# Kernel optimization log

Hardware: AMD Instinct MI355X
Metric: run time of the kernel (lower is better)

Reference implementation:

```python
import jax, jax.numpy as jnp
import numpy as np

K = 4  # number of conv kernel experts in CondConv_down


def setup_inputs() -> dict:
    key = jax.random.key(0)
    ks = jax.random.split(key, 8)
    N, Cin, H, W = 8, 64, 384, 384
    Cin2, Cout4, Cout2 = Cin // 2, 128 // 4, 128 // 2  # 32, 32, 64
    return {
        "x": jax.random.normal(ks[0], (N, Cin, H, W), jnp.float32),
        # square conv: Conv2d(in=64, out=64, 3x3, stride 2, pad 1, bias)
        "sq_w": jax.random.normal(ks[1], (Cout2, Cin, 3, 3), jnp.float32) * 0.05,
        "sq_b": jnp.zeros((Cout2,), jnp.float32),
        # vertical CondConv: attention 1x1 conv (== linear on pooled feats) + K expert kernels [3,1]
        "att_w_v": jax.random.normal(ks[2], (K, Cin2), jnp.float32) * 0.1,
        "att_b_v": jnp.zeros((K,), jnp.float32),
        "w_v": jax.random.normal(ks[3], (K, Cout4, Cin2, 3, 1), jnp.float32) * 0.05,
        "bn_v_g": jnp.ones((Cout4,), jnp.float32),
        "bn_v_b": jnp.zeros((Cout4,), jnp.float32),
        # horizontal CondConv: K expert kernels [1,3]
        "att_w_h": jax.random.normal(ks[4], (K, Cin2), jnp.float32) * 0.1,
        "att_b_h": jnp.zeros((K,), jnp.float32),
        "w_h": jax.random.normal(ks[5], (K, Cout4, Cin2, 1, 3), jnp.float32) * 0.05,
        "bn_h_g": jnp.ones((Cout4,), jnp.float32),
        "bn_h_b": jnp.zeros((Cout4,), jnp.float32),
    }


def _condconv(x, att_w, att_b, w, pad):
    # Attention: global avg pool -> 1x1 conv -> sigmoid (note: sigmoid, not softmax, as in source)
    att = jax.nn.sigmoid(jnp.mean(x, axis=(2, 3)) @ att_w.T + att_b)  # [N, K]
    # Aggregate expert kernels per sample: [N, Cout, Cin, kh, kw]
    agg = jnp.einsum("nk,koihw->noihw", att, w)
    def one(xi, wi):
        return jax.lax.conv_general_dilated(
            xi[None], wi, window_strides=(2, 2),
            padding=[(pad[0], pad[0]), (pad[1], pad[1])],
            dimension_numbers=("NCHW", "OIHW", "NCHW"))[0]
    return jax.vmap(one)(x, agg)  # per-sample dynamic conv == groups=N grouped conv


def _bn(x, g, b, eps=1e-5):
    # training-mode BatchNorm2d: batch statistics over (N, H, W), biased variance
    m = jnp.mean(x, axis=(0, 2, 3), keepdims=True)
    v = jnp.var(x, axis=(0, 2, 3), keepdims=True)
    return (x - m) * jax.lax.rsqrt(v + eps) * g[None, :, None, None] + b[None, :, None, None]


def _shuffle(x, g=8):
    N, C, H, W = x.shape
    return x.reshape(N, g, C // g, H, W).transpose(0, 2, 1, 3, 4).reshape(N, C, H, W)


def reference(x, sq_w, sq_b, att_w_v, att_b_v, w_v, bn_v_g, bn_v_b,
              att_w_h, att_b_h, w_h, bn_h_g, bn_h_b):
    sq = jax.lax.conv_general_dilated(
        x, sq_w, window_strides=(2, 2), padding=[(1, 1), (1, 1)],
        dimension_numbers=("NCHW", "OIHW", "NCHW")) + sq_b[None, :, None, None]
    x1, x2 = jnp.split(x, 2, axis=1)
    v = _bn(_condconv(x1, att_w_v, att_b_v, w_v, (1, 0)), bn_v_g, bn_v_b)
    h = _bn(_condconv(x2, att_w_h, att_b_h, w_h, (0, 1)), bn_h_g, bn_h_b)
    out = jnp.concatenate([sq, v, h], axis=1)  # [N, 128, H/2, W/2]
    return _shuffle(out, 8)
```

## Files before the change

### kernel.cpp

```cpp
#include <hip/hip_runtime.h>

#define NB    8
#define HIN   384
#define WIN   384
#define HOUT  192
#define WOUT  192
#define HW_IN (HIN * WIN)
#define PLANE (HOUT * WOUT)
#define CNT_BN (NB * HOUT * WOUT)

#define WS_MEANS 0
#define WS_AGGV  512
#define WS_AGGH  25088
#define WS_SQW   49664
#define WS_STATS 86528
#define WS_BN    86656

__global__ void k_zero(float* __restrict__ ws) {
    if (threadIdx.x < 128) ws[WS_STATS + threadIdx.x] = 0.f;
}

__global__ __launch_bounds__(256) void k_means(const float* __restrict__ x,
                                               float* __restrict__ ws) {
    int bc = blockIdx.x;
    const float4* p = (const float4*)(x + (size_t)bc * HW_IN);
    float s = 0.f;
    for (int i = threadIdx.x; i < HW_IN / 4; i += 256) {
        float4 v = p[i];
        s += (v.x + v.y) + (v.z + v.w);
    }
    __shared__ float red[256];
    red[threadIdx.x] = s;
    __syncthreads();
    for (int off = 128; off > 0; off >>= 1) {
        if ((int)threadIdx.x < off) red[threadIdx.x] += red[threadIdx.x + off];
        __syncthreads();
    }
    if (threadIdx.x == 0) ws[WS_MEANS + bc] = red[0] * (1.0f / HW_IN);
}

__global__ void k_agg(const float* __restrict__ aw_v, const float* __restrict__ ab_v,
                      const float* __restrict__ wv,
                      const float* __restrict__ aw_h, const float* __restrict__ ab_h,
                      const float* __restrict__ wh, float* __restrict__ ws) {
    int n = blockIdx.x;
    __shared__ float att[8];
    if (threadIdx.x < 8) {
        int k = threadIdx.x & 3;
        int hsel = threadIdx.x >> 2;
        const float* m = ws + WS_MEANS + n * 64 + hsel * 32;
        const float* aw = hsel ? aw_h : aw_v;
        const float* ab = hsel ? ab_h : ab_v;
        float z = ab[k];
        for (int c = 0; c < 32; c++) z += m[c] * aw[k * 32 + c];
        att[threadIdx.x] = 1.0f / (1.0f + expf(-z));
    }
    __syncthreads();
    for (int i = threadIdx.x; i < 3072; i += 256) {
        int o = i & 31;
        int r = i >> 5;
        float sv = 0.f, sh = 0.f;
#pragma unroll
        for (int k = 0; k < 4; k++) {
            sv += att[k]     * wv[(k * 32 + o) * 96 + r];
            sh += att[4 + k] * wh[(k * 32 + o) * 96 + r];
        }
        ws[WS_AGGV + n * 3072 + i] = sv;
        ws[WS_AGGH + n * 3072 + i] = sh;
    }
}

__global__ void k_cvtw(const float* __restrict__ sq_w, float* __restrict__ ws) {
    int i = blockIdx.x * 256 + threadIdx.x;
    int oc = i & 63;
    int r = i >> 6;
    int c = r / 9, q = r % 9;
    ws[WS_SQW + i] = sq_w[(oc * 64 + c) * 9 + q];
}

__global__ __launch_bounds__(192) void k_sq(const float* __restrict__ x,
                                            const float* __restrict__ sq_b,
                                            const float* __restrict__ ws,
                                            float* __restrict__ out) {
    int xo = threadIdx.x;
    int yo = blockIdx.x;
    int n  = blockIdx.y;
    int ocg = blockIdx.z;
    const float* wp = ws + WS_SQW + ocg * 32;
    const float* bptr = sq_b + ocg * 32;
    float acc[32];
#pragma unroll
    for (int j = 0; j < 32; j++) acc[j] = bptr[j];
    const float* xb = x + (size_t)n * 64 * HW_IN;
    int c2 = 2 * xo;
    for (int c = 0; c < 64; c++) {
        const float* xc = xb + (size_t)c * HW_IN;
#pragma unroll
        for (int ky = 0; ky < 3; ky++) {
            int iy = 2 * yo - 1 + ky;
            if (iy >= 0) {
                const float* row = xc + (size_t)iy * WIN;
                float2 v12 = *(const float2*)(row + c2);
                float v0 = (xo > 0) ? row[c2 - 1] : 0.f;
                const float* wr = wp + (c * 9 + ky * 3) * 64;
#pragma unroll
                for (int j = 0; j < 32; j++)
                    acc[j] += v0 * wr[j] + v12.x * wr[64 + j] + v12.y * wr[128 + j];
            }
        }
    }
    size_t ob = (size_t)n * 128 * PLANE + (size_t)yo * WOUT + xo;
#pragma unroll
    for (int j = 0; j < 32; j++) {
        int ci = ocg * 32 + j;
        int co = ((ci & 15) << 3) | (ci >> 4);
        out[ob + (size_t)co * PLANE] = acc[j];
    }
}

__global__ __launch_bounds__(192) void k_vert(const float* __restrict__ x,
                                              const float* __restrict__ ws,
                                              float* __restrict__ out) {
    int xo = threadIdx.x, yo = blockIdx.x, n = blockIdx.y;
    const float* wn = ws + WS_AGGV + n * 3072;
    float acc[32];
#pragma unroll
    for (int j = 0; j < 32; j++) acc[j] = 0.f;
    const float* xb = x + (size_t)n * 64 * HW_IN;
    int c2 = 2 * xo;
    for (int c = 0; c < 32; c++) {
        const float* xc = xb + (size_t)c * HW_IN;
#pragma unroll
        for (int t = 0; t < 3; t++) {
            int iy = 2 * yo - 1 + t;
            if (iy >= 0) {
                float v = xc[(size_t)iy * WIN + c2];
                const float* wr = wn + (c * 3 + t) * 32;
#pragma unroll
                for (int j = 0; j < 32; j++) acc[j] += v * wr[j];
            }
        }
    }
    size_t ob = (size_t)n * 128 * PLANE + (size_t)yo * WOUT + xo;
#pragma unroll
    for (int j = 0; j < 32; j++) {
        int ci = 64 + j;
        int co = ((ci & 15) << 3) | (ci >> 4);
        out[ob + (size_t)co * PLANE] = acc[j];
    }
}

__global__ __launch_bounds__(192) void k_horz(const float* __restrict__ x,
                                              const float* __restrict__ ws,
                                              float* __restrict__ out) {
    int xo = threadIdx.x, yo = blockIdx.x, n = blockIdx.y;
    const float* wn = ws + WS_AGGH + n * 3072;
    float acc[32];
#pragma unroll
    for (int j = 0; j < 32; j++) acc[j] = 0.f;
    const float* xb = x + ((size_t)n * 64 + 32) * HW_IN;
    int c2 = 2 * xo;
    for (int c = 0; c < 32; c++) {
        const float* row = xb + (size_t)c * HW_IN + (size_t)(2 * yo) * WIN;
        float2 v12 = *(const float2*)(row + c2);
        float v0 = (xo > 0) ? row[c2 - 1] : 0.f;
        const float* wr = wn + c * 96;
#pragma unroll
        for (int j = 0; j < 32; j++)
            acc[j] += v0 * wr[j] + v12.x * wr[32 + j] + v12.y * wr[64 + j];
    }
    size_t ob = (size_t)n * 128 * PLANE + (size_t)yo * WOUT + xo;
#pragma unroll
    for (int j = 0; j < 32; j++) {
        int ci = 96 + j;
        int co = ((ci & 15) << 3) | (ci >> 4);
        out[ob + (size_t)co * PLANE] = acc[j];
    }
}

__global__ __launch_bounds__(256) void k_stats(const float* __restrict__ out,
                                               float* __restrict__ ws) {
    int sch = blockIdx.x;
    int n = blockIdx.y;
    int vh = sch >> 5, oc = sch & 31;
    int ci = 64 + sch;
    int co = ((ci & 15) << 3) | (ci >> 4);
    const float4* p = (const float4*)(out + (size_t)(n * 128 + co) * PLANE);
    float s = 0.f, q = 0.f;
    for (int i = threadIdx.x; i < PLANE / 4; i += 256) {
        float4 v = p[i];
        s += (v.x + v.y) + (v.z + v.w);
        q += (v.x * v.x + v.y * v.y) + (v.z * v.z + v.w * v.w);
    }
    __shared__ float rs[256], rq[256];
    rs[threadIdx.x] = s; rq[threadIdx.x] = q;
    __syncthreads();
    for (int off = 128; off > 0; off >>= 1) {
        if ((int)threadIdx.x < off) {
            rs[threadIdx.x] += rs[threadIdx.x + off];
            rq[threadIdx.x] += rq[threadIdx.x + off];
        }
        __syncthreads();
    }
    if (threadIdx.x == 0) {
        atomicAdd(&ws[WS_STATS + vh * 64 + oc], rs[0]);
        atomicAdd(&ws[WS_STATS + vh * 64 + 32 + oc], rq[0]);
    }
}

__global__ void k_bnfin(const float* __restrict__ gv, const float* __restrict__ bv,
                        const float* __restrict__ gh, const float* __restrict__ bh,
                        float* __restrict__ ws) {
    int t = threadIdx.x;
    if (t >= 64) return;
    int vh = t >> 5;
    int c = t & 31;
    const float* st = ws + WS_STATS + vh * 64;
    float mean = st[c] * (1.0f / CNT_BN);
    float var = st[32 + c] * (1.0f / CNT_BN) - mean * mean;
    float g = vh ? gh[c] : gv[c];
    float b = vh ? bh[c] : bv[c];
    float scale = g * rsqrtf(var + 1e-5f);
    float* bn = ws + WS_BN + vh * 64;
    bn[c] = scale;
    bn[32 + c] = b - mean * scale;
}

__global__ __launch_bounds__(256) void k_apply(float* __restrict__ out,
                                               const float* __restrict__ ws) {
    int sch = blockIdx.x;
    int n = blockIdx.y;
    int vh = sch >> 5, oc = sch & 31;
    int ci = 64 + sch;
    int co = ((ci & 15) << 3) | (ci >> 4);
    const float* bn = ws + WS_BN + vh * 64;
    float scale = bn[oc], shift = bn[32 + oc];
    float4* p = (float4*)(out + (size_t)(n * 128 + co) * PLANE);
    for (int i = threadIdx.x; i < PLANE / 4; i += 256) {
        float4 v = p[i];
        v.x = v.x * scale + shift;
        v.y = v.y * scale + shift;
        v.z = v.z * scale + shift;
        v.w = v.w * scale + shift;
        p[i] = v;
    }
}

extern "C" void kernel_launch(void* const* d_in, const int* in_sizes, int n_in,
                              void* d_out, int out_size, void* d_ws, size_t ws_size,
                              hipStream_t stream) {
    const float* x    = (const float*)d_in[0];
    const float* sq_w = (const float*)d_in[1];
    const float* sq_b = (const float*)d_in[2];
    const float* aw_v = (const float*)d_in[3];
    const float* ab_v = (const float*)d_in[4];
    const float* w_v  = (const float*)d_in[5];
    const float* gv   = (const float*)d_in[6];
    const float* bv   = (const float*)d_in[7];
    const float* aw_h = (const float*)d_in[8];
    const float* ab_h = (const float*)d_in[9];
    const float* w_h  = (const float*)d_in[10];
    const float* gh   = (const float*)d_in[11];
    const float* bh   = (const float*)d_in[12];
    float* out = (float*)d_out;
    float* ws = (float*)d_ws;

    hipLaunchKernelGGL(k_zero, dim3(1), dim3(128), 0, stream, ws);
    hipLaunchKernelGGL(k_means, dim3(512), dim3(256), 0, stream, x, ws);
    hipLaunchKernelGGL(k_agg, dim3(8), dim3(256), 0, stream,
                       aw_v, ab_v, w_v, aw_h, ab_h, w_h, ws);
    hipLaunchKernelGGL(k_cvtw, dim3(144), dim3(256), 0, stream, sq_w, ws);
    hipLaunchKernelGGL(k_vert, dim3(192, 8), dim3(192), 0, stream, x, ws, out);
    hipLaunchKernelGGL(k_horz, dim3(192, 8), dim3(192), 0, stream, x, ws, out);
    hipLaunchKernelGGL(k_stats, dim3(64, 8), dim3(256), 0, stream, out, ws);
    hipLaunchKernelGGL(k_bnfin, dim3(1), dim3(64), 0, stream, gv, bv, gh, bh, ws);
    hipLaunchKernelGGL(k_apply, dim3(64, 8), dim3(256), 0, stream, out, ws);
    hipLaunchKernelGGL(k_sq, dim3(192, 8, 2), dim3(192), 0, stream, x, sq_b, ws, out);
}
```

Baseline: 948.2 us.

## Compute all 64 square-conv channels per thread, merge vert/horz kernels, split means

The square conv kernel now computes all 64 output channels per thread instead of two 32-channel groups. Each input pixel is loaded once, which halves reads of x, at the cost of 64 accumulators and more register pressure. The vertical and horizontal CondConv kernels are merged into one launch with a z-dimension selector, with unroll pragmas added. The channel-mean reduction is split into 4 parts per plane combined via atomicAdd, with scaling moved into k_agg, to expose more parallelism.

```diff
diff --git a/kernel.cpp b/kernel.cpp
--- a/kernel.cpp
+++ b/kernel.cpp
@@ -17,15 +17,17 @@
 #define WS_BN    86656
 
 __global__ void k_zero(float* __restrict__ ws) {
+    for (int i = threadIdx.x; i < 512; i += 256) ws[WS_MEANS + i] = 0.f;
     if (threadIdx.x < 128) ws[WS_STATS + threadIdx.x] = 0.f;
 }
 
 __global__ __launch_bounds__(256) void k_means(const float* __restrict__ x,
                                                float* __restrict__ ws) {
     int bc = blockIdx.x;
-    const float4* p = (const float4*)(x + (size_t)bc * HW_IN);
+    int part = blockIdx.y;
+    const float4* p = (const float4*)(x + (size_t)bc * HW_IN) + part * (HW_IN / 16);
     float s = 0.f;
-    for (int i = threadIdx.x; i < HW_IN / 4; i += 256) {
+    for (int i = threadIdx.x; i < HW_IN / 16; i += 256) {
         float4 v = p[i];
         s += (v.x + v.y) + (v.z + v.w);
     }
@@ -36,7 +38,7 @@
         if ((int)threadIdx.x < off) red[threadIdx.x] += red[threadIdx.x + off];
         __syncthreads();
     }
-    if (threadIdx.x == 0) ws[WS_MEANS + bc] = red[0] * (1.0f / HW_IN);
+    if (threadIdx.x == 0) atomicAdd(&ws[WS_MEANS + bc], red[0]);
 }
 
 __global__ void k_agg(const float* __restrict__ aw_v, const float* __restrict__ ab_v,
@@ -51,8 +53,9 @@
         const float* m = ws + WS_MEANS + n * 64 + hsel * 32;
         const float* aw = hsel ? aw_h : aw_v;
         const float* ab = hsel ? ab_h : ab_v;
-        float z = ab[k];
-        for (int c = 0; c < 32; c++) z += m[c] * aw[k * 32 + c];
+        float dot = 0.f;
+        for (int c = 0; c < 32; c++) dot += m[c] * aw[k * 32 + c];
+        float z = ab[k] + dot * (1.0f / HW_IN);
         att[threadIdx.x] = 1.0f / (1.0f + expf(-z));
     }
     __syncthreads();
@@ -85,94 +88,94 @@
     int xo = threadIdx.x;
     int yo = blockIdx.x;
     int n  = blockIdx.y;
-    int ocg = blockIdx.z;
-    const float* wp = ws + WS_SQW + ocg * 32;
-    const float* bptr = sq_b + ocg * 32;
-    float acc[32];
-#pragma unroll
-    for (int j = 0; j < 32; j++) acc[j] = bptr[j];
+    const float* wp = ws + WS_SQW;
+    float acc[64];
+#pragma unroll
+    for (int j = 0; j < 64; j++) acc[j] = sq_b[j];
     const float* xb = x + (size_t)n * 64 * HW_IN;
     int c2 = 2 * xo;
+    int iy0 = 2 * yo - 1;
     for (int c = 0; c < 64; c++) {
         const float* xc = xb + (size_t)c * HW_IN;
+        float v[9];
 #pragma unroll
         for (int ky = 0; ky < 3; ky++) {
-            int iy = 2 * yo - 1 + ky;
+            int iy = iy0 + ky;
             if (iy >= 0) {
                 const float* row = xc + (size_t)iy * WIN;
                 float2 v12 = *(const float2*)(row + c2);
-                float v0 = (xo > 0) ? row[c2 - 1] : 0.f;
-                const float* wr = wp + (c * 9 + ky * 3) * 64;
-#pragma unroll
-                for (int j = 0; j < 32; j++)
-                    acc[j] += v0 * wr[j] + v12.x * wr[64 + j] + v12.y * wr[128 + j];
+                v[ky * 3 + 0] = (xo > 0) ? row[c2 - 1] : 0.f;
+                v[ky * 3 + 1] = v12.x;
+                v[ky * 3 + 2] = v12.y;
+            } else {
+                v[ky * 3 + 0] = v[ky * 3 + 1] = v[ky * 3 + 2] = 0.f;
             }
         }
+        const float* wc = wp + c * 576;
+#pragma unroll
+        for (int t = 0; t < 9; t++) {
+            float vv = v[t];
+#pragma unroll
+            for (int j = 0; j < 64; j++) acc[j] += vv * wc[t * 64 + j];
+        }
     }
     size_t ob = (size_t)n * 128 * PLANE + (size_t)yo * WOUT + xo;
 #pragma unroll
+    for (int j = 0; j < 64; j++) {
+        int co = ((j & 15) << 3) | (j >> 4);
+        out[ob + (size_t)co * PLANE] = acc[j];
+    }
+}
+
+__global__ __launch_bounds__(192) void k_vh(const float* __restrict__ x,
+                                            const float* __restrict__ ws,
+                                            float* __restrict__ out) {
+    int xo = threadIdx.x, yo = blockIdx.x, n = blockIdx.y;
+    int horz = blockIdx.z;
+    float acc[32];
+#pragma unroll
+    for (int j = 0; j < 32; j++) acc[j] = 0.f;
+    if (!horz) {
+        const float* wn = ws + WS_AGGV + n * 3072;
+        const float* xb = x + (size_t)n * 64 * HW_IN;
+        int c2 = 2 * xo;
+        int iy0 = 2 * yo - 1;
+#pragma unroll 4
+        for (int c = 0; c < 32; c++) {
+            const float* xc = xb + (size_t)c * HW_IN;
+            float v[3];
+#pragma unroll
+            for (int t = 0; t < 3; t++) {
+                int iy = iy0 + t;
+                v[t] = (iy >= 0) ? xc[(size_t)iy * WIN + c2] : 0.f;
+            }
+#pragma unroll
+            for (int t = 0; t < 3; t++) {
+                const float* wr = wn + (c * 3 + t) * 32;
+#pragma unroll
+                for (int j = 0; j < 32; j++) acc[j] += v[t] * wr[j];
+            }
+        }
+    } else {
+        const float* wn = ws + WS_AGGH + n * 3072;
+        const float* xb = x + ((size_t)n * 64 + 32) * HW_IN;
+        int c2 = 2 * xo;
+#pragma unroll 4
+        for (int c = 0; c < 32; c++) {
+            const float* row = xb + (size_t)c * HW_IN + (size_t)(2 * yo) * WIN;
+            float2 v12 = *(const float2*)(row + c2);
+            float v0 = (xo > 0) ? row[c2 - 1] : 0.f;
+            const float* wr = wn + c * 96;
+#pragma unroll
+            for (int j = 0; j < 32; j++)
+                acc[j] += v0 * wr[j] + v12.x * wr[32 + j] + v12.y * wr[64 + j];
+        }
+    }
+    int cb = horz ? 96 : 64;
+    size_t ob = (size_t)n * 128 * PLANE + (size_t)yo * WOUT + xo;
+#pragma unroll
     for (int j = 0; j < 32; j++) {
-        int ci = ocg * 32 + j;
-        int co = ((ci & 15) << 3) | (ci >> 4);
-        out[ob + (size_t)co * PLANE] = acc[j];
-    }
-}
-
-__global__ __launch_bounds__(192) void k_vert(const float* __restrict__ x,
-                                              const float* __restrict__ ws,
-                                              float* __restrict__ out) {
-    int xo = threadIdx.x, yo = blockIdx.x, n = blockIdx.y;
-    const float* wn = ws + WS_AGGV + n * 3072;
-    float acc[32];
-#pragma unroll
-    for (int j = 0; j < 32; j++) acc[j] = 0.f;
-    const float* xb = x + (size_t)n * 64 * HW_IN;
-    int c2 = 2 * xo;
-    for (int c = 0; c < 32; c++) {
-        const float* xc = xb + (size_t)c * HW_IN;
-#pragma unroll
-        for (int t = 0; t < 3; t++) {
-            int iy = 2 * yo - 1 + t;
-            if (iy >= 0) {
-                float v = xc[(size_t)iy * WIN + c2];
-                const float* wr = wn + (c * 3 + t) * 32;
-#pragma unroll
-                for (int j = 0; j < 32; j++) acc[j] += v * wr[j];
-            }
-        }
-    }
-    size_t ob = (size_t)n * 128 * PLANE + (size_t)yo * WOUT + xo;
-#pragma unroll
-    for (int j = 0; j < 32; j++) {
-        int ci = 64 + j;
-        int co = ((ci & 15) << 3) | (ci >> 4);
-        out[ob + (size_t)co * PLANE] = acc[j];
-    }
-}
-
-__global__ __launch_bounds__(192) void k_horz(const float* __restrict__ x,
-                                              const float* __restrict__ ws,
-                                              float* __restrict__ out) {
-    int xo = threadIdx.x, yo = blockIdx.x, n = blockIdx.y;
-    const float* wn = ws + WS_AGGH + n * 3072;
-    float acc[32];
-#pragma unroll
-    for (int j = 0; j < 32; j++) acc[j] = 0.f;
-    const float* xb = x + ((size_t)n * 64 + 32) * HW_IN;
-    int c2 = 2 * xo;
-    for (int c = 0; c < 32; c++) {
-        const float* row = xb + (size_t)c * HW_IN + (size_t)(2 * yo) * WIN;
-        float2 v12 = *(const float2*)(row + c2);
-        float v0 = (xo > 0) ? row[c2 - 1] : 0.f;
-        const float* wr = wn + c * 96;
-#pragma unroll
-        for (int j = 0; j < 32; j++)
-            acc[j] += v0 * wr[j] + v12.x * wr[32 + j] + v12.y * wr[64 + j];
-    }
-    size_t ob = (size_t)n * 128 * PLANE + (size_t)yo * WOUT + xo;
-#pragma unroll
-    for (int j = 0; j < 32; j++) {
-        int ci = 96 + j;
+        int ci = cb + j;
         int co = ((ci & 15) << 3) | (ci >> 4);
         out[ob + (size_t)co * PLANE] = acc[j];
     }
@@ -265,15 +268,14 @@
     float* out = (float*)d_out;
     float* ws = (float*)d_ws;
 
-    hipLaunchKernelGGL(k_zero, dim3(1), dim3(128), 0, stream, ws);
-    hipLaunchKernelGGL(k_means, dim3(512), dim3(256), 0, stream, x, ws);
+    hipLaunchKernelGGL(k_zero, dim3(1), dim3(256), 0, stream, ws);
+    hipLaunchKernelGGL(k_means, dim3(512, 4), dim3(256), 0, stream, x, ws);
     hipLaunchKernelGGL(k_agg, dim3(8), dim3(256), 0, stream,
                        aw_v, ab_v, w_v, aw_h, ab_h, w_h, ws);
     hipLaunchKernelGGL(k_cvtw, dim3(144), dim3(256), 0, stream, sq_w, ws);
-    hipLaunchKernelGGL(k_vert, dim3(192, 8), dim3(192), 0, stream, x, ws, out);
-    hipLaunchKernelGGL(k_horz, dim3(192, 8), dim3(192), 0, stream, x, ws, out);
+    hipLaunchKernelGGL(k_vh, dim3(192, 8, 2), dim3(192), 0, stream, x, ws, out);
     hipLaunchKernelGGL(k_stats, dim3(64, 8), dim3(256), 0, stream, out, ws);
     hipLaunchKernelGGL(k_bnfin, dim3(1), dim3(64), 0, stream, gv, bv, gh, bh, ws);
     hipLaunchKernelGGL(k_apply, dim3(64, 8), dim3(256), 0, stream, out, ws);
-    hipLaunchKernelGGL(k_sq, dim3(192, 8, 2), dim3(192), 0, stream, x, sq_b, ws, out);
-}
+    hipLaunchKernelGGL(k_sq, dim3(192, 8), dim3(192), 0, stream, x, sq_b, ws, out);
+}
```

Result: slower. 999.0 us (+5.4%).
